# Optimization experiments

Measured on AMD Instinct MI355X. Metric: run time of the kernel, lower is better.

Reference implementation:

```python
import jax, jax.numpy as jnp
import numpy as np

N, E = 50000, 800000
F_IN, E_DIM, D, H = 128, 64, 64, 4  # per-head channels D, heads H; concat=False -> out dim D
GROUPS = 16
EPS = 1e-5


def _p(key, shape, scale):
    return (jax.random.normal(key, shape, dtype=jnp.float32) * scale)


def setup_inputs() -> dict:
    key = jax.random.key(0)
    ks = jax.random.split(key, 40)
    inp = {
        "x": jax.random.normal(ks[0], (N, F_IN), dtype=jnp.float32),
        "edge_index": jax.random.randint(ks[1], (2, E), 0, N, dtype=jnp.int64),
        "edge_attr": jax.random.normal(ks[2], (E, E_DIM), dtype=jnp.float32),
    }
    # TransformerConv params, layer i: Wq/Wk/Wv [in, H*D] (+bias), We [E_DIM, H*D] (no bias),
    # Wskip [in, D] (+bias).  Layer 1 in=F_IN, layers 2/3 in=D.
    idx = 3
    for i, fin in zip((1, 2, 3), (F_IN, D, D)):
        s = 1.0 / np.sqrt(fin)
        se = 1.0 / np.sqrt(E_DIM)
        inp[f"Wq{i}"] = _p(ks[idx + 0], (fin, H * D), s)
        inp[f"bq{i}"] = jnp.zeros((H * D,), jnp.float32)
        inp[f"Wk{i}"] = _p(ks[idx + 1], (fin, H * D), s)
        inp[f"bk{i}"] = jnp.zeros((H * D,), jnp.float32)
        inp[f"Wv{i}"] = _p(ks[idx + 2], (fin, H * D), s)
        inp[f"bv{i}"] = jnp.zeros((H * D,), jnp.float32)
        inp[f"We{i}"] = _p(ks[idx + 3], (E_DIM, H * D), se)
        inp[f"Wskip{i}"] = _p(ks[idx + 4], (fin, D), s)
        inp[f"bskip{i}"] = jnp.zeros((D,), jnp.float32)
        idx += 5
    inp["gn_w"] = jnp.ones((D,), jnp.float32)
    inp["gn_b"] = jnp.zeros((D,), jnp.float32)
    return inp


def transformer_conv(x, src, dst, edge_attr, Wq, bq, Wk, bk, Wv, bv, We, Wskip, bskip):
    n = x.shape[0]
    q = (x @ Wq + bq).reshape(n, H, D)
    k = (x @ Wk + bk).reshape(n, H, D)
    v = (x @ Wv + bv).reshape(n, H, D)
    e = (edge_attr @ We).reshape(-1, H, D)  # [E,H,D]
    k_e = k[src] + e                          # edge-level key
    v_e = v[src] + e                          # edge-level value
    alpha = jnp.einsum('ehd,ehd->eh', q[dst], k_e) / np.sqrt(D)  # [E,H]
    # segment softmax over incoming edges of each dst node
    amax = jax.ops.segment_max(alpha, dst, num_segments=n)
    amax = jnp.where(jnp.isfinite(amax), amax, 0.0)
    ex = jnp.exp(alpha - amax[dst])
    denom = jax.ops.segment_sum(ex, dst, num_segments=n)
    attn = ex / (denom[dst] + 1e-16)
    out = jax.ops.segment_sum(attn[:, :, None] * v_e, dst, num_segments=n)  # [N,H,D]
    out = out.mean(axis=1)                     # concat=False -> mean over heads
    return out + (x @ Wskip + bskip)           # root_weight skip


def group_norm(x, w, b):
    n, c = x.shape
    xg = x.reshape(n, GROUPS, c // GROUPS)
    mu = xg.mean(axis=2, keepdims=True)
    var = xg.var(axis=2, keepdims=True)
    xn = ((xg - mu) * jax.lax.rsqrt(var + EPS)).reshape(n, c)
    return xn * w + b


def reference(x, edge_index, edge_attr,
              Wq1, bq1, Wk1, bk1, Wv1, bv1, We1, Wskip1, bskip1,
              Wq2, bq2, Wk2, bk2, Wv2, bv2, We2, Wskip2, bskip2,
              Wq3, bq3, Wk3, bk3, Wv3, bv3, We3, Wskip3, bskip3,
              gn_w, gn_b):
    src, dst = edge_index[0], edge_index[1]
    layers = [
        (Wq1, bq1, Wk1, bk1, Wv1, bv1, We1, Wskip1, bskip1),
        (Wq2, bq2, Wk2, bk2, Wv2, bv2, We2, Wskip2, bskip2),
        (Wq3, bq3, Wk3, bk3, Wv3, bv3, We3, Wskip3, bskip3),
    ]
    h = x
    for prm in layers:
        h = transformer_conv(h, src, dst, edge_attr, *prm)
        h = group_norm(h, gn_w, gn_b)
        h = jax.nn.gelu(h, approximate=False)
    return h
```

## Files before the change

kernel.cpp:

```cpp
#include <hip/hip_runtime.h>
#include <math.h>

#define NN 50000
#define NE 800000
#define NCOLS 1088

typedef long long i64;

static __device__ __forceinline__ float4 ntl4(const float4* p) {
  typedef float f4v __attribute__((ext_vector_type(4)));
  f4v v = __builtin_nontemporal_load((const f4v*)p);
  float4 r; r.x = v.x; r.y = v.y; r.z = v.z; r.w = v.w;
  return r;
}
static __device__ __forceinline__ void nts4(float4* p, float4 a) {
  typedef float f4v __attribute__((ext_vector_type(4)));
  f4v v; v.x = a.x; v.y = a.y; v.z = a.z; v.w = a.w;
  __builtin_nontemporal_store(v, (f4v*)p);
}
static __device__ __forceinline__ void nts2(float* p, float a, float b) {
  typedef float f2v __attribute__((ext_vector_type(2)));
  f2v v; v.x = a; v.y = b;
  __builtin_nontemporal_store(v, (f2v*)p);
}

__global__ void detect_i64(const int* __restrict__ ei32, int* __restrict__ flag) {
  int i = blockIdx.x * blockDim.x + threadIdx.x;
  if (i < 2048) {
    if (ei32[2 * i + 1] != 0) atomicOr(flag, 1);
  }
}

__global__ void extract_edges(const void* __restrict__ ei, const int* __restrict__ flag,
                              int* __restrict__ src32, int* __restrict__ dst32, int ne) {
  int is32 = *flag;
  int i = blockIdx.x * blockDim.x + threadIdx.x;
  int st = gridDim.x * blockDim.x;
  if (is32) {
    const int* p = (const int*)ei;
    for (; i < ne; i += st) { src32[i] = p[i]; dst32[i] = p[ne + i]; }
  } else {
    const i64* p = (const i64*)ei;
    for (; i < ne; i += st) { src32[i] = (int)p[i]; dst32[i] = (int)p[ne + i]; }
  }
}

__global__ void hist_kernel(const int* __restrict__ dst, int* __restrict__ deg, int ne) {
  int i = blockIdx.x * blockDim.x + threadIdx.x;
  int st = gridDim.x * blockDim.x;
  for (; i < ne; i += st) atomicAdd(&deg[dst[i]], 1);
}

#define SCHUNK 1024
__global__ void scanA(const int* __restrict__ deg, int* __restrict__ row_ptr,
                      int* __restrict__ csum, int n) {
  __shared__ int buf[SCHUNK];
  int c = blockIdx.x, t = threadIdx.x;
  int idx = c * SCHUNK + t;
  int v = (idx < n) ? deg[idx] : 0;
  buf[t] = v;
  __syncthreads();
  for (int off = 1; off < SCHUNK; off <<= 1) {
    int x = (t >= off) ? buf[t - off] : 0;
    __syncthreads();
    buf[t] += x;
    __syncthreads();
  }
  if (idx < n) row_ptr[idx + 1] = buf[t];
  if (t == SCHUNK - 1) csum[c] = buf[t];
}

__global__ void scanB(int* __restrict__ csum, int nchunks) {
  if (threadIdx.x == 0 && blockIdx.x == 0) {
    int run = 0;
    for (int c = 0; c < nchunks; ++c) { int v = csum[c]; csum[c] = run; run += v; }
  }
}

__global__ void scanC(int* __restrict__ row_ptr, const int* __restrict__ csum, int n) {
  int c = blockIdx.x, t = threadIdx.x;
  int idx = c * SCHUNK + t;
  if (idx < n) row_ptr[idx + 1] += csum[c];
  if (idx == 0) row_ptr[0] = 0;
}

__global__ void scatter_kernel(const int* __restrict__ src, const int* __restrict__ dst,
                               const int* __restrict__ row_ptr, int* __restrict__ cursor,
                               int* __restrict__ src_sorted, int* __restrict__ eid_sorted, int ne) {
  int i = blockIdx.x * blockDim.x + threadIdx.x;
  int st = gridDim.x * blockDim.x;
  for (; i < ne; i += st) {
    int d = dst[i];
    int pos = row_ptr[d] + atomicAdd(&cursor[d], 1);
    src_sorted[pos] = src[i];
    eid_sorted[pos] = i;
  }
}

__global__ void sort_lists(const int* __restrict__ row_ptr, int* __restrict__ src_sorted,
                           int* __restrict__ eid_sorted, int n) {
  int node = blockIdx.x * blockDim.x + threadIdx.x;
  if (node >= n) return;
  int beg = row_ptr[node], end = row_ptr[node + 1];
  for (int a = beg + 1; a < end; ++a) {
    int e = eid_sorted[a], s = src_sorted[a];
    int b = a - 1;
    while (b >= beg && eid_sorted[b] > e) {
      eid_sorted[b + 1] = eid_sorted[b];
      src_sorted[b + 1] = src_sorted[b];
      --b;
    }
    eid_sorted[b + 1] = e; src_sorted[b + 1] = s;
  }
}

__global__ void ea_gather(const int* __restrict__ eid_sorted, const float* __restrict__ ea,
                          float* __restrict__ ea_csr, int ne) {
  long total = (long)ne * 16;
  long st = (long)gridDim.x * blockDim.x;
  for (long i = (long)blockIdx.x * blockDim.x + threadIdx.x; i < total; i += st) {
    int j = (int)(i >> 4);
    int c = (int)(i & 15);
    int e = eid_sorted[j];
    float4 v = ntl4(((const float4*)ea) + (size_t)e * 16 + c);
    nts4(((float4*)ea_csr) + i, v);
  }
}

__global__ void prep_wt(const float* __restrict__ Wq, const float* __restrict__ Wk,
                        const float* __restrict__ Wv, const float* __restrict__ We,
                        const float* __restrict__ Wsk, float* __restrict__ Wt, int fin) {
  int i = blockIdx.x * blockDim.x + threadIdx.x;
  if (i >= NCOLS * fin) return;
  int col = i / fin, k = i % fin;
  float val;
  if (col < 768) {
    const float* W = (col < 256) ? Wq : (col < 512) ? Wk : Wv;
    val = W[k * 256 + (col & 255)];
  } else if (col < 1024) {
    int idx = col - 768; int h = idx >> 6, ce = idx & 63;
    float a = 0.f;
    for (int d = 0; d < 64; ++d) a += Wq[k * 256 + h * 64 + d] * We[ce * 256 + h * 64 + d];
    val = a;
  } else {
    val = Wsk[k * 64 + (col - 1024)];
  }
  Wt[(size_t)col * fin + k] = val;
}

__global__ void prep_bias(const float* __restrict__ bq, const float* __restrict__ bk,
                          const float* __restrict__ bv, const float* __restrict__ We,
                          const float* __restrict__ bsk, float* __restrict__ bb) {
  int col = blockIdx.x * blockDim.x + threadIdx.x;
  if (col >= NCOLS) return;
  float val;
  if (col < 768) {
    const float* b = (col < 256) ? bq : (col < 512) ? bk : bv;
    val = b[col & 255];
  } else if (col < 1024) {
    int idx = col - 768; int h = idx >> 6, ce = idx & 63;
    float a = 0.f;
    for (int d = 0; d < 64; ++d) a += bq[h * 64 + d] * We[ce * 256 + h * 64 + d];
    val = a;
  } else {
    val = bsk[col - 1024];
  }
  bb[col] = val;
}

__global__ __launch_bounds__(256) void node_gemm_f32(
    const float* __restrict__ X, const float* __restrict__ Wt, const float* __restrict__ bb,
    float* __restrict__ qq_tab, float* __restrict__ kv_tab,
    float* __restrict__ skip_tab, int n, int fin) {
  __shared__ __align__(16) float Xs[128][68];
  __shared__ __align__(16) float Ws[64][68];
  int tid = threadIdx.x;
  int tx = tid & 15, ty = tid >> 4;
  int m0 = blockIdx.x * 128, c0 = blockIdx.y * 64;
  float acc[8][4];
  #pragma unroll
  for (int i = 0; i < 8; ++i)
    #pragma unroll
    for (int j = 0; j < 4; ++j) acc[i][j] = 0.f;

  for (int k0 = 0; k0 < fin; k0 += 64) {
    #pragma unroll
    for (int p = 0; p < 8; ++p) {
      int r = ty + 16 * p;
      float4 xv = make_float4(0.f, 0.f, 0.f, 0.f);
      if (m0 + r < n) xv = *(const float4*)&X[(size_t)(m0 + r) * fin + k0 + tx * 4];
      *(float4*)&Xs[r][tx * 4] = xv;
    }
    #pragma unroll
    for (int p = 0; p < 4; ++p) {
      int r = ty + 16 * p;
      float4 wv = *(const float4*)&Wt[(size_t)(c0 + r) * fin + k0 + tx * 4];
      *(float4*)&Ws[r][tx * 4] = wv;
    }
    __syncthreads();
    #pragma unroll 4
    for (int kk = 0; kk < 64; kk += 4) {
      float4 a[8], b[4];
      #pragma unroll
      for (int i = 0; i < 8; ++i) a[i] = *(const float4*)&Xs[ty + 16 * i][kk];
      #pragma unroll
      for (int j = 0; j < 4; ++j) b[j] = *(const float4*)&Ws[tx + 16 * j][kk];
      #pragma unroll
      for (int i = 0; i < 8; ++i)
        #pragma unroll
        for (int j = 0; j < 4; ++j) {
          acc[i][j] = fmaf(a[i].x, b[j].x, acc[i][j]);
          acc[i][j] = fmaf(a[i].y, b[j].y, acc[i][j]);
          acc[i][j] = fmaf(a[i].z, b[j].z, acc[i][j]);
          acc[i][j] = fmaf(a[i].w, b[j].w, acc[i][j]);
        }
    }
    __syncthreads();
  }
  #pragma unroll
  for (int j = 0; j < 4; ++j) {
    int col = c0 + tx + 16 * j;
    float bias = bb[col];
    #pragma unroll
    for (int i = 0; i < 8; ++i) {
      int row = m0 + ty + 16 * i;
      if (row >= n) continue;
      float val = acc[i][j] + bias;
      if (col < 256)        qq_tab[(size_t)row * 512 + col] = val;
      else if (col < 768)   kv_tab[(size_t)row * 512 + col - 256] = val;
      else if (col < 1024)  qq_tab[(size_t)row * 512 + col - 512] = val;
      else                  skip_tab[(size_t)row * 64 + col - 1024] = val;
    }
  }
}

__global__ __launch_bounds__(256) void attn_kernel_v5(
    const int* __restrict__ row_ptr, const int* __restrict__ src_sorted,
    const int* __restrict__ eid_sorted, const float* __restrict__ ea,
    const float* __restrict__ ea_csr, int use_csr,
    const float* __restrict__ qq_tab, const float* __restrict__ kv_tab,
    const float* __restrict__ skip_tab, const float* __restrict__ west,
    const float* __restrict__ gnw, const float* __restrict__ gnb,
    float* __restrict__ out, int n) {
  int tid = threadIdx.x;
  int wave = tid >> 6, lane = tid & 63;
  int half = lane >> 5, h = (lane >> 3) & 3, c8 = lane & 7;
  int ko = h * 16 + c8 * 2;
  int eo = c8 * 2;
  const float4* qq4 = (const float4*)qq_tab;
  const float4* kv4 = (const float4*)kv_tab;
  const float4* e4p = (const float4*)ea;
  const float4* ec4 = (const float4*)ea_csr;
  const float4* w4p = (const float4*)west;

  int node = blockIdx.x * 8 + wave * 2 + half;
  int beg = 0, deg = 0;
  if (node < n) {
    beg = row_ptr[node];
    deg = row_ptr[node + 1] - beg;
  } else {
    node = -1;
  }
  int tmax = deg;
  { int o = __shfl_xor(tmax, 32); tmax = o > tmax ? o : tmax; }

  float4 q4a = make_float4(0.f,0.f,0.f,0.f), q4b = q4a, t4a = q4a, t4b = q4a;
  if (node >= 0) {
    q4a = ntl4(&qq4[(size_t)node * 128 + ko]);
    q4b = ntl4(&qq4[(size_t)node * 128 + ko + 1]);
    t4a = ntl4(&qq4[(size_t)node * 128 + 64 + ko]);
    t4b = ntl4(&qq4[(size_t)node * 128 + 64 + ko + 1]);
  }

  float m = -INFINITY, s = 0.f;
  float4 av0 = make_float4(0.f,0.f,0.f,0.f), av1 = av0, aw0 = av0, aw1 = av0;

#define LOADP(jdx, K0r, K1r, V0r, V1r, E0r, E1r)              \
  {                                                           \
    int jc = (jdx); if (jc > NE - 1) jc = NE - 1;             \
    int s_ = src_sorted[jc];                                  \
    const float4* kr = kv4 + (size_t)s_ * 128;                \
    K0r = kr[ko]; K1r = kr[ko + 1];                           \
    V0r = kr[64 + ko]; V1r = kr[64 + ko + 1];                 \
    if (use_csr) {                                            \
      const float4* er = ec4 + (size_t)jc * 16;               \
      E0r = ntl4(er + eo); E1r = ntl4(er + eo + 1);           \
    } else {                                                  \
      int e_ = eid_sorted[jc];                                \
      const float4* er = e4p + (size_t)e_ * 16;               \
      E0r = ntl4(er + eo); E1r = ntl4(er + eo + 1);           \
    }                                                         \
  }

#define SCORE_ONLINE(tt, K0, K1, V0, V1, E0, E1)              \
  {                                                           \
    float p = q4a.x * K0.x + q4a.y * K0.y + q4a.z * K0.z + q4a.w * K0.w; \
    p = fmaf(q4b.x, K1.x, p); p = fmaf(q4b.y, K1.y, p);       \
    p = fmaf(q4b.z, K1.z, p); p = fmaf(q4b.w, K1.w, p);       \
    p = fmaf(t4a.x, E0.x, p); p = fmaf(t4a.y, E0.y, p);       \
    p = fmaf(t4a.z, E0.z, p); p = fmaf(t4a.w, E0.w, p);       \
    p = fmaf(t4b.x, E1.x, p); p = fmaf(t4b.y, E1.y, p);       \
    p = fmaf(t4b.z, E1.z, p); p = fmaf(t4b.w, E1.w, p);       \
    p += __shfl_xor(p, 1);                                    \
    p += __shfl_xor(p, 2);                                    \
    p += __shfl_xor(p, 4);                                    \
    p *= 0.125f;                                              \
    bool valid = ((tt) < deg);                                \
    float d_ = p - m;                                         \
    float e_ = __expf(-fabsf(d_));                            \
    float sc = (valid && d_ > 0.f) ? e_ : 1.f;                \
    float pp = valid ? ((d_ > 0.f) ? 1.f : e_) : 0.f;         \
    if (valid) m = fmaxf(m, p);                               \
    s = s * sc + pp;                                          \
    av0.x = av0.x * sc + pp * V0.x; av0.y = av0.y * sc + pp * V0.y; \
    av0.z = av0.z * sc + pp * V0.z; av0.w = av0.w * sc + pp * V0.w; \
    av1.x = av1.x * sc + pp * V1.x; av1.y = av1.y * sc + pp * V1.y; \
    av1.z = av1.z * sc + pp * V1.z; av1.w = av1.w * sc + pp * V1.w; \
    aw0.x = aw0.x * sc + pp * E0.x; aw0.y = aw0.y * sc + pp * E0.y; \
    aw0.z = aw0.z * sc + pp * E0.z; aw0.w = aw0.w * sc + pp * E0.w; \
    aw1.x = aw1.x * sc + pp * E1.x; aw1.y = aw1.y * sc + pp * E1.y; \
    aw1.z = aw1.z * sc + pp * E1.z; aw1.w = aw1.w * sc + pp * E1.w; \
  }

  float4 KA0, KA1, VA0, VA1, EA0, EA1;
  float4 KB0, KB1, VB0, VB1, EB0, EB1;
  LOADP(beg + 0, KA0, KA1, VA0, VA1, EA0, EA1);
  LOADP(beg + 1, KB0, KB1, VB0, VB1, EB0, EB1);

  for (int t = 0; t < tmax; t += 2) {
    {
      float4 nK0, nK1, nV0, nV1, nE0, nE1;
      LOADP(beg + t + 2, nK0, nK1, nV0, nV1, nE0, nE1);
      SCORE_ONLINE(t, KA0, KA1, VA0, VA1, EA0, EA1);
      KA0 = nK0; KA1 = nK1; VA0 = nV0; VA1 = nV1; EA0 = nE0; EA1 = nE1;
    }
    if (t + 1 < tmax) {
      float4 nK0, nK1, nV0, nV1, nE0, nE1;
      LOADP(beg + t + 3, nK0, nK1, nV0, nV1, nE0, nE1);
      SCORE_ONLINE(t + 1, KB0, KB1, VB0, VB1, EB0, EB1);
      KB0 = nK0; KB1 = nK1; VB0 = nV0; VB1 = nV1; EB0 = nE0; EB1 = nE1;
    }
  }

  float inv = s > 0.f ? 1.f / s : 0.f;
  float4 avn0 = make_float4(av0.x*inv, av0.y*inv, av0.z*inv, av0.w*inv);
  float4 avn1 = make_float4(av1.x*inv, av1.y*inv, av1.z*inv, av1.w*inv);
  float4 awn0 = make_float4(aw0.x*inv, aw0.y*inv, aw0.z*inv, aw0.w*inv);
  float4 awn1 = make_float4(aw1.x*inv, aw1.y*inv, aw1.z*inv, aw1.w*inv);

  float4 post0 = make_float4(0.f,0.f,0.f,0.f), post1 = post0;
  int lbase = lane & 0x38;
  #pragma unroll
  for (int cc4 = 0; cc4 < 16; ++cc4) {
    float4 srcv = (cc4 & 1) ? awn1 : awn0;
    int sl = lbase | (cc4 >> 1);
    float wa = __shfl(srcv.x, sl);
    float wb = __shfl(srcv.y, sl);
    float wc = __shfl(srcv.z, sl);
    float wd = __shfl(srcv.w, sl);
    const float4* wr = w4p + (size_t)(cc4 * 4) * 64 + ko;
    float4 wA0 = wr[0],   wA1 = wr[1];
    float4 wB0 = wr[64],  wB1 = wr[65];
    float4 wC0 = wr[128], wC1 = wr[129];
    float4 wD0 = wr[192], wD1 = wr[193];
    post0.x = fmaf(wa, wA0.x, post0.x); post0.y = fmaf(wa, wA0.y, post0.y);
    post0.z = fmaf(wa, wA0.z, post0.z); post0.w = fmaf(wa, wA0.w, post0.w);
    post1.x = fmaf(wa, wA1.x, post1.x); post1.y = fmaf(wa, wA1.y, post1.y);
    post1.z = fmaf(wa, wA1.z, post1.z); post1.w = fmaf(wa, wA1.w, post1.w);
    post0.x = fmaf(wb, wB0.x, post0.x); post0.y = fmaf(wb, wB0.y, post0.y);
    post0.z = fmaf(wb, wB0.z, post0.z); post0.w = fmaf(wb, wB0.w, post0.w);
    post1.x = fmaf(wb, wB1.x, post1.x); post1.y = fmaf(wb, wB1.y, post1.y);
    post1.z = fmaf(wb, wB1.z, post1.z); post1.w = fmaf(wb, wB1.w, post1.w);
    post0.x = fmaf(wc, wC0.x, post0.x); post0.y = fmaf(wc, wC0.y, post0.y);
    post0.z = fmaf(wc, wC0.z, post0.z); post0.w = fmaf(wc, wC0.w, post0.w);
    post1.x = fmaf(wc, wC1.x, post1.x); post1.y = fmaf(wc, wC1.y, post1.y);
    post1.z = fmaf(wc, wC1.z, post1.z); post1.w = fmaf(wc, wC1.w, post1.w);
    post0.x = fmaf(wd, wD0.x, post0.x); post0.y = fmaf(wd, wD0.y, post0.y);
    post0.z = fmaf(wd, wD0.z, post0.z); post0.w = fmaf(wd, wD0.w, post0.w);
    post1.x = fmaf(wd, wD1.x, post1.x); post1.y = fmaf(wd, wD1.y, post1.y);
    post1.z = fmaf(wd, wD1.z, post1.z); post1.w = fmaf(wd, wD1.w, post1.w);
  }

  float4 tot0 = make_float4(avn0.x+post0.x, avn0.y+post0.y, avn0.z+post0.z, avn0.w+post0.w);
  float4 tot1 = make_float4(avn1.x+post1.x, avn1.y+post1.y, avn1.z+post1.z, avn1.w+post1.w);
  tot0.x += __shfl_xor(tot0.x, 8);  tot0.y += __shfl_xor(tot0.y, 8);
  tot0.z += __shfl_xor(tot0.z, 8);  tot0.w += __shfl_xor(tot0.w, 8);
  tot1.x += __shfl_xor(tot1.x, 8);  tot1.y += __shfl_xor(tot1.y, 8);
  tot1.z += __shfl_xor(tot1.z, 8);  tot1.w += __shfl_xor(tot1.w, 8);
  tot0.x += __shfl_xor(tot0.x, 16); tot0.y += __shfl_xor(tot0.y, 16);
  tot0.z += __shfl_xor(tot0.z, 16); tot0.w += __shfl_xor(tot0.w, 16);
  tot1.x += __shfl_xor(tot1.x, 16); tot1.y += __shfl_xor(tot1.y, 16);
  tot1.z += __shfl_xor(tot1.z, 16); tot1.w += __shfl_xor(tot1.w, 16);

  if (node >= 0) {
    const float4* skr = (const float4*)(skip_tab + (size_t)node * 64);
    float4 sk0 = ntl4(&skr[c8 * 2]), sk1 = ntl4(&skr[c8 * 2 + 1]);
    const float4* gwr = (const float4*)gnw;
    const float4* gbr = (const float4*)gnb;
    float4 gw0 = gwr[c8 * 2], gw1 = gwr[c8 * 2 + 1];
    float4 gb0 = gbr[c8 * 2], gb1 = gbr[c8 * 2 + 1];
    float a0 = 0.25f * tot0.x + sk0.x, a1 = 0.25f * tot0.y + sk0.y;
    float a2 = 0.25f * tot0.z + sk0.z, a3 = 0.25f * tot0.w + sk0.w;
    float b0 = 0.25f * tot1.x + sk1.x, b1 = 0.25f * tot1.y + sk1.y;
    float b2 = 0.25f * tot1.z + sk1.z, b3 = 0.25f * tot1.w + sk1.w;
    float muA = ((a0 + a1) + (a2 + a3)) * 0.25f;
    float muB = ((b0 + b1) + (b2 + b3)) * 0.25f;
    float dA0 = a0-muA, dA1 = a1-muA, dA2 = a2-muA, dA3 = a3-muA;
    float dB0 = b0-muB, dB1 = b1-muB, dB2 = b2-muB, dB3 = b3-muB;
    float vA = ((dA0*dA0 + dA1*dA1) + (dA2*dA2 + dA3*dA3)) * 0.25f;
    float vB = ((dB0*dB0 + dB1*dB1) + (dB2*dB2 + dB3*dB3)) * 0.25f;
    float rA = rsqrtf(vA + 1e-5f), rB = rsqrtf(vB + 1e-5f);
    float yA0 = dA0*rA*gw0.x + gb0.x, yA1 = dA1*rA*gw0.y + gb0.y;
    float yA2 = dA2*rA*gw0.z + gb0.z, yA3 = dA3*rA*gw0.w + gb0.w;
    float yB0 = dB0*rB*gw1.x + gb1.x, yB1 = dB1*rB*gw1.y + gb1.y;
    float yB2 = dB2*rB*gw1.z + gb1.z, yB3 = dB3*rB*gw1.w + gb1.w;
    #define GELU(y) (0.5f * (y) * (1.0f + erff((y) * 0.70710678118654752f)))
    float gA0 = GELU(yA0), gA1 = GELU(yA1), gA2 = GELU(yA2), gA3 = GELU(yA3);
    float gB0 = GELU(yB0), gB1 = GELU(yB1), gB2 = GELU(yB2), gB3 = GELU(yB3);
    float ox, oy;
    if (h == 0)      { ox = gA0; oy = gA1; }
    else if (h == 1) { ox = gA2; oy = gA3; }
    else if (h == 2) { ox = gB0; oy = gB1; }
    else             { ox = gB2; oy = gB3; }
    nts2(out + (size_t)node * 64 + c8 * 8 + h * 2, ox, oy);
  }
}

extern "C" void kernel_launch(void* const* d_in, const int* in_sizes, int n_in,
                              void* d_out, int out_size, void* d_ws, size_t ws_size,
                              hipStream_t stream) {
  (void)in_sizes; (void)n_in;
  const float* x = (const float*)d_in[0];
  const void* ei = d_in[1];
  const float* ea = (const float*)d_in[2];
  const float *Wq[3], *bq[3], *Wk[3], *bk[3], *Wv[3], *bv[3], *We[3], *Wsk[3], *bsk[3];
  for (int L = 0; L < 3; ++L) {
    int b = 3 + 9 * L;
    Wq[L] = (const float*)d_in[b + 0]; bq[L] = (const float*)d_in[b + 1];
    Wk[L] = (const float*)d_in[b + 2]; bk[L] = (const float*)d_in[b + 3];
    Wv[L] = (const float*)d_in[b + 4]; bv[L] = (const float*)d_in[b + 5];
    We[L] = (const float*)d_in[b + 6]; Wsk[L] = (const float*)d_in[b + 7];
    bsk[L] = (const float*)d_in[b + 8];
  }
  const float* gnw = (const float*)d_in[30];
  const float* gnb = (const float*)d_in[31];

  char* p = (char*)d_ws;
  auto alloc = [&](size_t bytes) -> void* {
    void* r = (void*)p;
    p += (bytes + 255) & ~(size_t)255;
    return r;
  };
  float* qq_tab = (float*)alloc((size_t)NN * 512 * 4);
  float* kv_tab = (float*)alloc((size_t)NN * 512 * 4);
  float* skip_tab = (float*)alloc((size_t)NN * 64 * 4);
  float* h_buf = (float*)alloc((size_t)NN * 64 * 4);
  int* row_ptr = (int*)alloc((size_t)(NN + 1) * 4);
  int* deg = (int*)alloc((size_t)NN * 4);
  int* cursor = (int*)alloc((size_t)NN * 4);
  int* csum = (int*)alloc(1024 * 4);
  int* src_sorted = (int*)alloc((size_t)NE * 4);
  int* eid_sorted = (int*)alloc((size_t)NE * 4);
  int* src32 = (int*)alloc((size_t)NE * 4);
  int* dst32 = (int*)alloc((size_t)NE * 4);
  int* flag = (int*)alloc(256);
  float* Wt[3]; float* bb[3];
  Wt[0] = (float*)alloc((size_t)NCOLS * 128 * 4);
  Wt[1] = (float*)alloc((size_t)NCOLS * 64 * 4);
  Wt[2] = (float*)alloc((size_t)NCOLS * 64 * 4);
  for (int L = 0; L < 3; ++L) bb[L] = (float*)alloc((size_t)NCOLS * 4);

  if ((size_t)(p - (char*)d_ws) > ws_size) {
    hipMemsetAsync(d_out, 0, (size_t)out_size * 4, stream);
    return;
  }

  float* ea_csr = nullptr;
  int use_csr = 0;
  {
    size_t need = (size_t)(p - (char*)d_ws) + (size_t)NE * 64 * 4 + 256;
    if (need <= ws_size) {
      ea_csr = (float*)alloc((size_t)NE * 64 * 4);
      use_csr = 1;
    }
  }

  hipMemsetAsync(deg, 0, (size_t)NN * 4, stream);
  hipMemsetAsync(cursor, 0, (size_t)NN * 4, stream);
  hipMemsetAsync(flag, 0, 4, stream);

  detect_i64<<<8, 256, 0, stream>>>((const int*)ei, flag);
  extract_edges<<<2048, 256, 0, stream>>>(ei, flag, src32, dst32, NE);

  hist_kernel<<<2048, 256, 0, stream>>>(dst32, deg, NE);
  int nchunks = (NN + SCHUNK - 1) / SCHUNK;
  scanA<<<nchunks, SCHUNK, 0, stream>>>(deg, row_ptr, csum, NN);
  scanB<<<1, 64, 0, stream>>>(csum, nchunks);
  scanC<<<nchunks, SCHUNK, 0, stream>>>(row_ptr, csum, NN);
  scatter_kernel<<<2048, 256, 0, stream>>>(src32, dst32, row_ptr, cursor, src_sorted, eid_sorted, NE);
  sort_lists<<<(NN + 255) / 256, 256, 0, stream>>>(row_ptr, src_sorted, eid_sorted, NN);
  if (use_csr)
    ea_gather<<<2048, 256, 0, stream>>>(eid_sorted, ea, ea_csr, NE);

  for (int L = 0; L < 3; ++L) {
    int fin = (L == 0) ? 128 : 64;
    prep_wt<<<(NCOLS * fin + 255) / 256, 256, 0, stream>>>(Wq[L], Wk[L], Wv[L], We[L], Wsk[L], Wt[L], fin);
    prep_bias<<<(NCOLS + 255) / 256, 256, 0, stream>>>(bq[L], bk[L], bv[L], We[L], bsk[L], bb[L]);
  }

  const float* hin = x;
  int nblk = (NN + 7) / 8;
  for (int L = 0; L < 3; ++L) {
    int fin = (L == 0) ? 128 : 64;
    dim3 g((NN + 127) / 128, 17);
    node_gemm_f32<<<g, 256, 0, stream>>>(hin, Wt[L], bb[L], qq_tab, kv_tab, skip_tab, NN, fin);
    attn_kernel_v5<<<nblk, 256, 0, stream>>>(
        row_ptr, src_sorted, eid_sorted, ea, ea_csr, use_csr, qq_tab, kv_tab,
        skip_tab, We[L], gnw, gnb,
        (L == 2) ? (float*)d_out : h_buf, NN);
    hin = h_buf;
  }
}
```

Measured before the change: 1.886 ms.

## Split attention epilogue into separate post-GEMM and finish kernels, one node per wave

Restructures each layer's attention stage into three kernels. The aggregation kernel now assigns one node per wave instead of two per wave, has each lane hold one float4 of K/V/E, and writes the normalized edge-attribute aggregate to a new table. A tiled GEMM then applies We per head, and a third kernel does the skip add, GroupNorm and GELU. The aim is to take the per-lane We projection, with its many shuffles and weight loads, out of the latency-bound gather loop and to drop the nontemporal hints. The cost is extra kernel launches and an N×256 intermediate round trip through memory.

After: 1.761 ms. 6.6% less time.

```diff
diff --git a/kernel.cpp b/kernel.cpp
--- a/kernel.cpp
+++ b/kernel.cpp
@@ -6,23 +6,6 @@
 #define NCOLS 1088
 
 typedef long long i64;
-
-static __device__ __forceinline__ float4 ntl4(const float4* p) {
-  typedef float f4v __attribute__((ext_vector_type(4)));
-  f4v v = __builtin_nontemporal_load((const f4v*)p);
-  float4 r; r.x = v.x; r.y = v.y; r.z = v.z; r.w = v.w;
-  return r;
-}
-static __device__ __forceinline__ void nts4(float4* p, float4 a) {
-  typedef float f4v __attribute__((ext_vector_type(4)));
-  f4v v; v.x = a.x; v.y = a.y; v.z = a.z; v.w = a.w;
-  __builtin_nontemporal_store(v, (f4v*)p);
-}
-static __device__ __forceinline__ void nts2(float* p, float a, float b) {
-  typedef float f2v __attribute__((ext_vector_type(2)));
-  f2v v; v.x = a; v.y = b;
-  __builtin_nontemporal_store(v, (f2v*)p);
-}
 
 __global__ void detect_i64(const int* __restrict__ ei32, int* __restrict__ flag) {
   int i = blockIdx.x * blockDim.x + threadIdx.x;
@@ -122,8 +105,7 @@
     int j = (int)(i >> 4);
     int c = (int)(i & 15);
     int e = eid_sorted[j];
-    float4 v = ntl4(((const float4*)ea) + (size_t)e * 16 + c);
-    nts4(((float4*)ea_csr) + i, v);
+    ((float4*)ea_csr)[i] = ((const float4*)ea)[(size_t)e * 16 + c];
   }
 }
 
@@ -168,6 +150,14 @@
   bb[col] = val;
 }
 
+__global__ void prep_wpost(const float* __restrict__ We, float* __restrict__ Wt2) {
+  int i = blockIdx.x * blockDim.x + threadIdx.x;
+  if (i >= 64 * 256) return;
+  int col = i >> 8, k = i & 255;
+  int h = k >> 6, ce = k & 63;
+  Wt2[i] = We[ce * 256 + h * 64 + col];
+}
+
 __global__ __launch_bounds__(256) void node_gemm_f32(
     const float* __restrict__ X, const float* __restrict__ Wt, const float* __restrict__ bb,
     float* __restrict__ qq_tab, float* __restrict__ kv_tab,
@@ -228,202 +218,193 @@
       float val = acc[i][j] + bias;
       if (col < 256)        qq_tab[(size_t)row * 512 + col] = val;
       else if (col < 768)   kv_tab[(size_t)row * 512 + col - 256] = val;
-      else if (col < 1024)  qq_tab[(size_t)row * 512 + col - 512] = val;
+      else if (col < 1024)  qq_tab[(size_t)row * 512 + col - 768 + 256] = val;
       else                  skip_tab[(size_t)row * 64 + col - 1024] = val;
     }
   }
 }
 
-__global__ __launch_bounds__(256) void attn_kernel_v5(
+__global__ __launch_bounds__(256) void post_gemm(
+    const float* __restrict__ A, const float* __restrict__ B, float* __restrict__ C, int n) {
+  __shared__ __align__(16) float Xs[128][68];
+  __shared__ __align__(16) float Ws[64][68];
+  int tid = threadIdx.x;
+  int tx = tid & 15, ty = tid >> 4;
+  int m0 = blockIdx.x * 128;
+  float acc[8][4];
+  #pragma unroll
+  for (int i = 0; i < 8; ++i)
+    #pragma unroll
+    for (int j = 0; j < 4; ++j) acc[i][j] = 0.f;
+
+  for (int k0 = 0; k0 < 256; k0 += 64) {
+    #pragma unroll
+    for (int p = 0; p < 8; ++p) {
+      int r = ty + 16 * p;
+      float4 xv = make_float4(0.f, 0.f, 0.f, 0.f);
+      if (m0 + r < n) xv = *(const float4*)&A[(size_t)(m0 + r) * 256 + k0 + tx * 4];
+      *(float4*)&Xs[r][tx * 4] = xv;
+    }
+    #pragma unroll
+    for (int p = 0; p < 4; ++p) {
+      int r = ty + 16 * p;
+      float4 wv = *(const float4*)&B[(size_t)r * 256 + k0 + tx * 4];
+      *(float4*)&Ws[r][tx * 4] = wv;
+    }
+    __syncthreads();
+    #pragma unroll 4
+    for (int kk = 0; kk < 64; kk += 4) {
+      float4 a[8], b[4];
+      #pragma unroll
+      for (int i = 0; i < 8; ++i) a[i] = *(const float4*)&Xs[ty + 16 * i][kk];
+      #pragma unroll
+      for (int j = 0; j < 4; ++j) b[j] = *(const float4*)&Ws[tx + 16 * j][kk];
+      #pragma unroll
+      for (int i = 0; i < 8; ++i)
+        #pragma unroll
+        for (int j = 0; j < 4; ++j) {
+          acc[i][j] = fmaf(a[i].x, b[j].x, acc[i][j]);
+          acc[i][j] = fmaf(a[i].y, b[j].y, acc[i][j]);
+          acc[i][j] = fmaf(a[i].z, b[j].z, acc[i][j]);
+          acc[i][j] = fmaf(a[i].w, b[j].w, acc[i][j]);
+        }
+    }
+    __syncthreads();
+  }
+  #pragma unroll
+  for (int j = 0; j < 4; ++j) {
+    int col = tx + 16 * j;
+    #pragma unroll
+    for (int i = 0; i < 8; ++i) {
+      int row = m0 + ty + 16 * i;
+      if (row >= n) continue;
+      C[(size_t)row * 64 + col] = acc[i][j];
+    }
+  }
+}
+
+__global__ __launch_bounds__(256) void attn_kernel_v6(
     const int* __restrict__ row_ptr, const int* __restrict__ src_sorted,
     const int* __restrict__ eid_sorted, const float* __restrict__ ea,
     const float* __restrict__ ea_csr, int use_csr,
     const float* __restrict__ qq_tab, const float* __restrict__ kv_tab,
-    const float* __restrict__ skip_tab, const float* __restrict__ west,
-    const float* __restrict__ gnw, const float* __restrict__ gnb,
-    float* __restrict__ out, int n) {
+    float* __restrict__ avs_tab, float* __restrict__ awn_tab, int n) {
   int tid = threadIdx.x;
   int wave = tid >> 6, lane = tid & 63;
-  int half = lane >> 5, h = (lane >> 3) & 3, c8 = lane & 7;
-  int ko = h * 16 + c8 * 2;
-  int eo = c8 * 2;
+  int c16 = lane & 15;
   const float4* qq4 = (const float4*)qq_tab;
   const float4* kv4 = (const float4*)kv_tab;
+  const float4* ec4 = (const float4*)ea_csr;
   const float4* e4p = (const float4*)ea;
-  const float4* ec4 = (const float4*)ea_csr;
-  const float4* w4p = (const float4*)west;
-
-  int node = blockIdx.x * 8 + wave * 2 + half;
-  int beg = 0, deg = 0;
-  if (node < n) {
-    beg = row_ptr[node];
-    deg = row_ptr[node + 1] - beg;
-  } else {
-    node = -1;
-  }
-  int tmax = deg;
-  { int o = __shfl_xor(tmax, 32); tmax = o > tmax ? o : tmax; }
-
-  float4 q4a = make_float4(0.f,0.f,0.f,0.f), q4b = q4a, t4a = q4a, t4b = q4a;
-  if (node >= 0) {
-    q4a = ntl4(&qq4[(size_t)node * 128 + ko]);
-    q4b = ntl4(&qq4[(size_t)node * 128 + ko + 1]);
-    t4a = ntl4(&qq4[(size_t)node * 128 + 64 + ko]);
-    t4b = ntl4(&qq4[(size_t)node * 128 + 64 + ko + 1]);
-  }
+
+  int node = blockIdx.x * 4 + wave;
+  if (node >= n) return;
+  int beg = row_ptr[node];
+  int deg = row_ptr[node + 1] - beg;
+
+  float4 q4 = qq4[(size_t)node * 128 + lane];
+  float4 t4 = qq4[(size_t)node * 128 + 64 + lane];
 
   float m = -INFINITY, s = 0.f;
-  float4 av0 = make_float4(0.f,0.f,0.f,0.f), av1 = av0, aw0 = av0, aw1 = av0;
-
-#define LOADP(jdx, K0r, K1r, V0r, V1r, E0r, E1r)              \
+  float4 av = make_float4(0.f, 0.f, 0.f, 0.f);
+  float4 aw = make_float4(0.f, 0.f, 0.f, 0.f);
+
+#define LDE(j_, K_, V_, E_)                                   \
   {                                                           \
-    int jc = (jdx); if (jc > NE - 1) jc = NE - 1;             \
+    int jc = (j_); int jm = beg + deg - 1;                    \
+    if (jc > jm) jc = jm;                                     \
     int s_ = src_sorted[jc];                                  \
     const float4* kr = kv4 + (size_t)s_ * 128;                \
-    K0r = kr[ko]; K1r = kr[ko + 1];                           \
-    V0r = kr[64 + ko]; V1r = kr[64 + ko + 1];                 \
-    if (use_csr) {                                            \
-      const float4* er = ec4 + (size_t)jc * 16;               \
-      E0r = ntl4(er + eo); E1r = ntl4(er + eo + 1);           \
-    } else {                                                  \
-      int e_ = eid_sorted[jc];                                \
-      const float4* er = e4p + (size_t)e_ * 16;               \
-      E0r = ntl4(er + eo); E1r = ntl4(er + eo + 1);           \
-    }                                                         \
-  }
-
-#define SCORE_ONLINE(tt, K0, K1, V0, V1, E0, E1)              \
+    K_ = kr[lane]; V_ = kr[64 + lane];                        \
+    if (use_csr) E_ = ec4[(size_t)jc * 16 + c16];             \
+    else { int e_ = eid_sorted[jc];                           \
+           E_ = e4p[(size_t)e_ * 16 + c16]; }                 \
+  }
+
+#define PROC(K_, V_, E_)                                      \
   {                                                           \
-    float p = q4a.x * K0.x + q4a.y * K0.y + q4a.z * K0.z + q4a.w * K0.w; \
-    p = fmaf(q4b.x, K1.x, p); p = fmaf(q4b.y, K1.y, p);       \
-    p = fmaf(q4b.z, K1.z, p); p = fmaf(q4b.w, K1.w, p);       \
-    p = fmaf(t4a.x, E0.x, p); p = fmaf(t4a.y, E0.y, p);       \
-    p = fmaf(t4a.z, E0.z, p); p = fmaf(t4a.w, E0.w, p);       \
-    p = fmaf(t4b.x, E1.x, p); p = fmaf(t4b.y, E1.y, p);       \
-    p = fmaf(t4b.z, E1.z, p); p = fmaf(t4b.w, E1.w, p);       \
+    float p = q4.x * K_.x + q4.y * K_.y + q4.z * K_.z + q4.w * K_.w \
+            + t4.x * E_.x + t4.y * E_.y + t4.z * E_.z + t4.w * E_.w; \
     p += __shfl_xor(p, 1);                                    \
     p += __shfl_xor(p, 2);                                    \
     p += __shfl_xor(p, 4);                                    \
+    p += __shfl_xor(p, 8);                                    \
     p *= 0.125f;                                              \
-    bool valid = ((tt) < deg);                                \
     float d_ = p - m;                                         \
     float e_ = __expf(-fabsf(d_));                            \
-    float sc = (valid && d_ > 0.f) ? e_ : 1.f;                \
-    float pp = valid ? ((d_ > 0.f) ? 1.f : e_) : 0.f;         \
-    if (valid) m = fmaxf(m, p);                               \
+    float sc = d_ > 0.f ? e_ : 1.f;                           \
+    float pp = d_ > 0.f ? 1.f : e_;                           \
+    m = fmaxf(m, p);                                          \
     s = s * sc + pp;                                          \
-    av0.x = av0.x * sc + pp * V0.x; av0.y = av0.y * sc + pp * V0.y; \
-    av0.z = av0.z * sc + pp * V0.z; av0.w = av0.w * sc + pp * V0.w; \
-    av1.x = av1.x * sc + pp * V1.x; av1.y = av1.y * sc + pp * V1.y; \
-    av1.z = av1.z * sc + pp * V1.z; av1.w = av1.w * sc + pp * V1.w; \
-    aw0.x = aw0.x * sc + pp * E0.x; aw0.y = aw0.y * sc + pp * E0.y; \
-    aw0.z = aw0.z * sc + pp * E0.z; aw0.w = aw0.w * sc + pp * E0.w; \
-    aw1.x = aw1.x * sc + pp * E1.x; aw1.y = aw1.y * sc + pp * E1.y; \
-    aw1.z = aw1.z * sc + pp * E1.z; aw1.w = aw1.w * sc + pp * E1.w; \
-  }
-
-  float4 KA0, KA1, VA0, VA1, EA0, EA1;
-  float4 KB0, KB1, VB0, VB1, EB0, EB1;
-  LOADP(beg + 0, KA0, KA1, VA0, VA1, EA0, EA1);
-  LOADP(beg + 1, KB0, KB1, VB0, VB1, EB0, EB1);
-
-  for (int t = 0; t < tmax; t += 2) {
-    {
-      float4 nK0, nK1, nV0, nV1, nE0, nE1;
-      LOADP(beg + t + 2, nK0, nK1, nV0, nV1, nE0, nE1);
-      SCORE_ONLINE(t, KA0, KA1, VA0, VA1, EA0, EA1);
-      KA0 = nK0; KA1 = nK1; VA0 = nV0; VA1 = nV1; EA0 = nE0; EA1 = nE1;
-    }
-    if (t + 1 < tmax) {
-      float4 nK0, nK1, nV0, nV1, nE0, nE1;
-      LOADP(beg + t + 3, nK0, nK1, nV0, nV1, nE0, nE1);
-      SCORE_ONLINE(t + 1, KB0, KB1, VB0, VB1, EB0, EB1);
-      KB0 = nK0; KB1 = nK1; VB0 = nV0; VB1 = nV1; EB0 = nE0; EB1 = nE1;
-    }
+    av.x = av.x * sc + pp * V_.x; av.y = av.y * sc + pp * V_.y; \
+    av.z = av.z * sc + pp * V_.z; av.w = av.w * sc + pp * V_.w; \
+    aw.x = aw.x * sc + pp * E_.x; aw.y = aw.y * sc + pp * E_.y; \
+    aw.z = aw.z * sc + pp * E_.z; aw.w = aw.w * sc + pp * E_.w; \
+  }
+
+  if (deg > 0) {
+    float4 KA, VA, EA, KB, VB, EB;
+    LDE(beg + 0, KA, VA, EA);
+    LDE(beg + 1, KB, VB, EB);
+    int t = 0;
+    for (; t + 1 < deg; t += 2) {
+      {
+        float4 nK, nV, nE;
+        LDE(beg + t + 2, nK, nV, nE);
+        PROC(KA, VA, EA);
+        KA = nK; VA = nV; EA = nE;
+      }
+      {
+        float4 nK, nV, nE;
+        LDE(beg + t + 3, nK, nV, nE);
+        PROC(KB, VB, EB);
+        KB = nK; VB = nV; EB = nE;
+      }
+    }
+    if (t < deg) PROC(KA, VA, EA);
   }
 
   float inv = s > 0.f ? 1.f / s : 0.f;
-  float4 avn0 = make_float4(av0.x*inv, av0.y*inv, av0.z*inv, av0.w*inv);
-  float4 avn1 = make_float4(av1.x*inv, av1.y*inv, av1.z*inv, av1.w*inv);
-  float4 awn0 = make_float4(aw0.x*inv, aw0.y*inv, aw0.z*inv, aw0.w*inv);
-  float4 awn1 = make_float4(aw1.x*inv, aw1.y*inv, aw1.z*inv, aw1.w*inv);
-
-  float4 post0 = make_float4(0.f,0.f,0.f,0.f), post1 = post0;
-  int lbase = lane & 0x38;
-  #pragma unroll
-  for (int cc4 = 0; cc4 < 16; ++cc4) {
-    float4 srcv = (cc4 & 1) ? awn1 : awn0;
-    int sl = lbase | (cc4 >> 1);
-    float wa = __shfl(srcv.x, sl);
-    float wb = __shfl(srcv.y, sl);
-    float wc = __shfl(srcv.z, sl);
-    float wd = __shfl(srcv.w, sl);
-    const float4* wr = w4p + (size_t)(cc4 * 4) * 64 + ko;
-    float4 wA0 = wr[0],   wA1 = wr[1];
-    float4 wB0 = wr[64],  wB1 = wr[65];
-    float4 wC0 = wr[128], wC1 = wr[129];
-    float4 wD0 = wr[192], wD1 = wr[193];
-    post0.x = fmaf(wa, wA0.x, post0.x); post0.y = fmaf(wa, wA0.y, post0.y);
-    post0.z = fmaf(wa, wA0.z, post0.z); post0.w = fmaf(wa, wA0.w, post0.w);
-    post1.x = fmaf(wa, wA1.x, post1.x); post1.y = fmaf(wa, wA1.y, post1.y);
-    post1.z = fmaf(wa, wA1.z, post1.z); post1.w = fmaf(wa, wA1.w, post1.w);
-    post0.x = fmaf(wb, wB0.x, post0.x); post0.y = fmaf(wb, wB0.y, post0.y);
-    post0.z = fmaf(wb, wB0.z, post0.z); post0.w = fmaf(wb, wB0.w, post0.w);
-    post1.x = fmaf(wb, wB1.x, post1.x); post1.y = fmaf(wb, wB1.y, post1.y);
-    post1.z = fmaf(wb, wB1.z, post1.z); post1.w = fmaf(wb, wB1.w, post1.w);
-    post0.x = fmaf(wc, wC0.x, post0.x); post0.y = fmaf(wc, wC0.y, post0.y);
-    post0.z = fmaf(wc, wC0.z, post0.z); post0.w = fmaf(wc, wC0.w, post0.w);
-    post1.x = fmaf(wc, wC1.x, post1.x); post1.y = fmaf(wc, wC1.y, post1.y);
-    post1.z = fmaf(wc, wC1.z, post1.z); post1.w = fmaf(wc, wC1.w, post1.w);
-    post0.x = fmaf(wd, wD0.x, post0.x); post0.y = fmaf(wd, wD0.y, post0.y);
-    post0.z = fmaf(wd, wD0.z, post0.z); post0.w = fmaf(wd, wD0.w, post0.w);
-    post1.x = fmaf(wd, wD1.x, post1.x); post1.y = fmaf(wd, wD1.y, post1.y);
-    post1.z = fmaf(wd, wD1.z, post1.z); post1.w = fmaf(wd, wD1.w, post1.w);
-  }
-
-  float4 tot0 = make_float4(avn0.x+post0.x, avn0.y+post0.y, avn0.z+post0.z, avn0.w+post0.w);
-  float4 tot1 = make_float4(avn1.x+post1.x, avn1.y+post1.y, avn1.z+post1.z, avn1.w+post1.w);
-  tot0.x += __shfl_xor(tot0.x, 8);  tot0.y += __shfl_xor(tot0.y, 8);
-  tot0.z += __shfl_xor(tot0.z, 8);  tot0.w += __shfl_xor(tot0.w, 8);
-  tot1.x += __shfl_xor(tot1.x, 8);  tot1.y += __shfl_xor(tot1.y, 8);
-  tot1.z += __shfl_xor(tot1.z, 8);  tot1.w += __shfl_xor(tot1.w, 8);
-  tot0.x += __shfl_xor(tot0.x, 16); tot0.y += __shfl_xor(tot0.y, 16);
-  tot0.z += __shfl_xor(tot0.z, 16); tot0.w += __shfl_xor(tot0.w, 16);
-  tot1.x += __shfl_xor(tot1.x, 16); tot1.y += __shfl_xor(tot1.y, 16);
-  tot1.z += __shfl_xor(tot1.z, 16); tot1.w += __shfl_xor(tot1.w, 16);
-
-  if (node >= 0) {
-    const float4* skr = (const float4*)(skip_tab + (size_t)node * 64);
-    float4 sk0 = ntl4(&skr[c8 * 2]), sk1 = ntl4(&skr[c8 * 2 + 1]);
-    const float4* gwr = (const float4*)gnw;
-    const float4* gbr = (const float4*)gnb;
-    float4 gw0 = gwr[c8 * 2], gw1 = gwr[c8 * 2 + 1];
-    float4 gb0 = gbr[c8 * 2], gb1 = gbr[c8 * 2 + 1];
-    float a0 = 0.25f * tot0.x + sk0.x, a1 = 0.25f * tot0.y + sk0.y;
-    float a2 = 0.25f * tot0.z + sk0.z, a3 = 0.25f * tot0.w + sk0.w;
-    float b0 = 0.25f * tot1.x + sk1.x, b1 = 0.25f * tot1.y + sk1.y;
-    float b2 = 0.25f * tot1.z + sk1.z, b3 = 0.25f * tot1.w + sk1.w;
-    float muA = ((a0 + a1) + (a2 + a3)) * 0.25f;
-    float muB = ((b0 + b1) + (b2 + b3)) * 0.25f;
-    float dA0 = a0-muA, dA1 = a1-muA, dA2 = a2-muA, dA3 = a3-muA;
-    float dB0 = b0-muB, dB1 = b1-muB, dB2 = b2-muB, dB3 = b3-muB;
-    float vA = ((dA0*dA0 + dA1*dA1) + (dA2*dA2 + dA3*dA3)) * 0.25f;
-    float vB = ((dB0*dB0 + dB1*dB1) + (dB2*dB2 + dB3*dB3)) * 0.25f;
-    float rA = rsqrtf(vA + 1e-5f), rB = rsqrtf(vB + 1e-5f);
-    float yA0 = dA0*rA*gw0.x + gb0.x, yA1 = dA1*rA*gw0.y + gb0.y;
-    float yA2 = dA2*rA*gw0.z + gb0.z, yA3 = dA3*rA*gw0.w + gb0.w;
-    float yB0 = dB0*rB*gw1.x + gb1.x, yB1 = dB1*rB*gw1.y + gb1.y;
-    float yB2 = dB2*rB*gw1.z + gb1.z, yB3 = dB3*rB*gw1.w + gb1.w;
-    #define GELU(y) (0.5f * (y) * (1.0f + erff((y) * 0.70710678118654752f)))
-    float gA0 = GELU(yA0), gA1 = GELU(yA1), gA2 = GELU(yA2), gA3 = GELU(yA3);
-    float gB0 = GELU(yB0), gB1 = GELU(yB1), gB2 = GELU(yB2), gB3 = GELU(yB3);
-    float ox, oy;
-    if (h == 0)      { ox = gA0; oy = gA1; }
-    else if (h == 1) { ox = gA2; oy = gA3; }
-    else if (h == 2) { ox = gB0; oy = gB1; }
-    else             { ox = gB2; oy = gB3; }
-    nts2(out + (size_t)node * 64 + c8 * 8 + h * 2, ox, oy);
-  }
+  float4 awn = make_float4(aw.x * inv, aw.y * inv, aw.z * inv, aw.w * inv);
+  float4 avn = make_float4(av.x * inv, av.y * inv, av.z * inv, av.w * inv);
+
+  ((float4*)awn_tab)[(size_t)node * 64 + lane] = awn;
+
+  avn.x += __shfl_xor(avn.x, 16); avn.y += __shfl_xor(avn.y, 16);
+  avn.z += __shfl_xor(avn.z, 16); avn.w += __shfl_xor(avn.w, 16);
+  avn.x += __shfl_xor(avn.x, 32); avn.y += __shfl_xor(avn.y, 32);
+  avn.z += __shfl_xor(avn.z, 32); avn.w += __shfl_xor(avn.w, 32);
+  if (lane < 16)
+    ((float4*)avs_tab)[(size_t)node * 16 + c16] = avn;
+}
+
+__global__ void finish_kernel(const float* __restrict__ avs, const float* __restrict__ post,
+                              const float* __restrict__ skip, const float* __restrict__ gnw,
+                              const float* __restrict__ gnb, float* __restrict__ out, int n) {
+  int g = blockIdx.x * blockDim.x + threadIdx.x;
+  if (g >= n * 16) return;
+  int node = g >> 4, grp = g & 15;
+  float4 a = ((const float4*)avs)[(size_t)node * 16 + grp];
+  float4 p = ((const float4*)post)[(size_t)node * 16 + grp];
+  float4 sk = ((const float4*)skip)[(size_t)node * 16 + grp];
+  float4 gw = ((const float4*)gnw)[grp];
+  float4 gb = ((const float4*)gnb)[grp];
+  float v0 = 0.25f * (a.x + p.x) + sk.x;
+  float v1 = 0.25f * (a.y + p.y) + sk.y;
+  float v2 = 0.25f * (a.z + p.z) + sk.z;
+  float v3 = 0.25f * (a.w + p.w) + sk.w;
+  float mu = ((v0 + v1) + (v2 + v3)) * 0.25f;
+  float d0 = v0 - mu, d1 = v1 - mu, d2 = v2 - mu, d3 = v3 - mu;
+  float var = ((d0 * d0 + d1 * d1) + (d2 * d2 + d3 * d3)) * 0.25f;
+  float r = rsqrtf(var + 1e-5f);
+  float y0 = d0 * r * gw.x + gb.x;
+  float y1 = d1 * r * gw.y + gb.y;
+  float y2 = d2 * r * gw.z + gb.z;
+  float y3 = d3 * r * gw.w + gb.w;
+  #define GELU(y) (0.5f * (y) * (1.0f + erff((y) * 0.70710678118654752f)))
+  float4 o;
+  o.x = GELU(y0); o.y = GELU(y1); o.z = GELU(y2); o.w = GELU(y3);
+  ((float4*)out)[(size_t)node * 16 + grp] = o;
 }
 
 extern "C" void kernel_launch(void* const* d_in, const int* in_sizes, int n_in,
@@ -455,6 +436,9 @@
   float* kv_tab = (float*)alloc((size_t)NN * 512 * 4);
   float* skip_tab = (float*)alloc((size_t)NN * 64 * 4);
   float* h_buf = (float*)alloc((size_t)NN * 64 * 4);
+  float* avs_tab = (float*)alloc((size_t)NN * 64 * 4);
+  float* awn_tab = (float*)alloc((size_t)NN * 256 * 4);
+  float* post_tab = (float*)alloc((size_t)NN * 64 * 4);
   int* row_ptr = (int*)alloc((size_t)(NN + 1) * 4);
   int* deg = (int*)alloc((size_t)NN * 4);
   int* cursor = (int*)alloc((size_t)NN * 4);
@@ -464,11 +448,12 @@
   int* src32 = (int*)alloc((size_t)NE * 4);
   int* dst32 = (int*)alloc((size_t)NE * 4);
   int* flag = (int*)alloc(256);
-  float* Wt[3]; float* bb[3];
+  float* Wt[3]; float* bb[3]; float* Wt2[3];
   Wt[0] = (float*)alloc((size_t)NCOLS * 128 * 4);
   Wt[1] = (float*)alloc((size_t)NCOLS * 64 * 4);
   Wt[2] = (float*)alloc((size_t)NCOLS * 64 * 4);
   for (int L = 0; L < 3; ++L) bb[L] = (float*)alloc((size_t)NCOLS * 4);
+  for (int L = 0; L < 3; ++L) Wt2[L] = (float*)alloc((size_t)64 * 256 * 4);
 
   if ((size_t)(p - (char*)d_ws) > ws_size) {
     hipMemsetAsync(d_out, 0, (size_t)out_size * 4, stream);
@@ -506,17 +491,21 @@
     int fin = (L == 0) ? 128 : 64;
     prep_wt<<<(NCOLS * fin + 255) / 256, 256, 0, stream>>>(Wq[L], Wk[L], Wv[L], We[L], Wsk[L], Wt[L], fin);
     prep_bias<<<(NCOLS + 255) / 256, 256, 0, stream>>>(bq[L], bk[L], bv[L], We[L], bsk[L], bb[L]);
+    prep_wpost<<<64, 256, 0, stream>>>(We[L], Wt2[L]);
   }
 
   const float* hin = x;
-  int nblk = (NN + 7) / 8;
+  int nblk = (NN + 3) / 4;
   for (int L = 0; L < 3; ++L) {
     int fin = (L == 0) ? 128 : 64;
     dim3 g((NN + 127) / 128, 17);
     node_gemm_f32<<<g, 256, 0, stream>>>(hin, Wt[L], bb[L], qq_tab, kv_tab, skip_tab, NN, fin);
-    attn_kernel_v5<<<nblk, 256, 0, stream>>>(
-        row_ptr, src_sorted, eid_sorted, ea, ea_csr, use_csr, qq_tab, kv_tab,
-        skip_tab, We[L], gnw, gnb,
+    attn_kernel_v6<<<nblk, 256, 0, stream>>>(
+        row_ptr, src_sorted, eid_sorted, ea, ea_csr, use_csr,
+        qq_tab, kv_tab, avs_tab, awn_tab, NN);
+    post_gemm<<<(NN + 127) / 128, 256, 0, stream>>>(awn_tab, Wt2[L], post_tab, NN);
+    finish_kernel<<<(NN * 16 + 255) / 256, 256, 0, stream>>>(
+        avs_tab, post_tab, skip_tab, gnw, gnb,
         (L == 2) ? (float*)d_out : h_buf, NN);
     hin = h_buf;
   }
```
